# Performance work log

Hardware: AMD Instinct MI355X
Metric: run time of the kernel (lower is better)

Reference implementation:

```python
import jax, jax.numpy as jnp
import numpy as np
from jax import lax

# dims: batch, depth, height, width, in-channels
B, D, H, W, C = 1, 48, 48, 48, 8
K = 3          # cubic kernel size
R = 2          # n_radial_profiles = K//2 + 1
DEG = 3        # max_degree
NH = (DEG + 1) ** 2   # n_harmonics = 16
OUT = 16       # out_channels (filters)


def setup_inputs() -> dict:
    key = jax.random.key(0)
    ks = jax.random.split(key, 6)
    return {
        "x": jax.random.normal(ks[0], (B, D, H, W, C), jnp.float32),
        "atoms_real": jax.random.normal(ks[1], (K, K, K, R, NH), jnp.float32),
        "atoms_imag": jax.random.normal(ks[2], (K, K, K, R, NH), jnp.float32),
        "w": jax.random.normal(ks[3], (C, OUT, R, DEG + 1), jnp.float32) * 0.1,
        "w_center": jax.random.normal(ks[4], (C, OUT), jnp.float32) * 0.1,
        "b_center": jnp.zeros((OUT,), jnp.float32),
    }


def _depthwise_sh_conv(x, filt):
    # x: [B,D,H,W,C]; filt: [K,K,K,R,NH].  The torch code loops conv3d per input
    # channel with the SAME [K,K,K,1,R*NH] filter bank; that is exactly a
    # depthwise conv with channel multiplier R*NH and a tiled kernel.
    k = filt.shape[0]
    r, nh = filt.shape[3], filt.shape[4]
    c = x.shape[-1]
    kern = jnp.tile(filt.reshape(k, k, k, 1, r * nh), (1, 1, 1, 1, c))  # [K,K,K,1,C*R*NH], c-major
    dn = lax.conv_dimension_numbers(x.shape, kern.shape, ("NDHWC", "DHWIO", "NDHWC"))
    y = lax.conv_general_dilated(x, kern, (1, 1, 1), "SAME",
                                 dimension_numbers=dn, feature_group_count=c)
    # -> [B,D,H,W,C,R,NH]
    return y.reshape(x.shape[:4] + (c, r, nh))


def reference(x, atoms_real, atoms_imag, w, w_center, b_center):
    deg = w.shape[-1] - 1
    # repeat_interleave of per-degree weights over the 2k+1 orders of each degree
    idx = np.repeat(np.arange(deg + 1), [2 * n + 1 for n in range(deg + 1)])  # [NH]
    w_exp = w[..., idx]  # [C, OUT, R, NH]

    feat_r = _depthwise_sh_conv(x, atoms_real)  # [B,D,H,W,C,R,NH]
    feat_i = _depthwise_sh_conv(x, atoms_imag)

    # weighted reduction over input channels (axis 4) and radial profiles (axis 6)
    real = jnp.einsum("bdhwcrn,cfrn->bdhwfn", feat_r, w_exp)
    imag = jnp.einsum("bdhwcrn,cfrn->bdhwfn", feat_i, w_exp)

    # central-pixel 1x1x1 conv added to harmonic index 0 of the real part
    central = jnp.einsum("bdhwc,cf->bdhwf", x, w_center) + b_center
    real = real.at[..., 0].add(central)

    # stack real/imag feature maps: [B,D,H,W,OUT,NH,2]
    return jnp.stack([real, imag], axis=-1)
```

## Files before the change

### kernel.cpp

```cpp
#include <hip/hip_runtime.h>


typedef _Float16 half4_t __attribute__((ext_vector_type(4)));
typedef float floatx4 __attribute__((ext_vector_type(4)));

#define B_U64_SLOTS (14 * 32 * 64)
#define WS_BYTES_NEEDED (B_U64_SLOTS * 8)

__device__ inline unsigned short f2h(float v) {
    return __builtin_bit_cast(unsigned short, (_Float16)v);
}
__device__ inline unsigned pk2(float a, float b) {
    return (unsigned)f2h(a) | ((unsigned)f2h(b) << 16);
}

__global__ __launch_bounds__(512) void bsh_precompute_gemm(
    const float* __restrict__ AR,
    const float* __restrict__ AI,
    const float* __restrict__ Wgt,
    const float* __restrict__ WC,
    const float* __restrict__ Bc,
    unsigned long long* __restrict__ TB)
{
    int s = blockIdx.x * 512 + threadIdx.x;
    if (s >= B_U64_SLOTS) return;
    int l = s & 63, ntg = (s >> 6) & 31, t = s >> 11;
    int col = 16 * ntg + (l & 15);
    int f = col >> 5, n = (col >> 1) & 15, ri = col & 1;
    int dg = (n >= 9) ? 3 : (n >= 4) ? 2 : (n >= 1) ? 1 : 0;
    const float* atom = ri ? AI : AR;
    unsigned long long pack = 0;
    #pragma unroll
    for (int j = 0; j < 4; ++j) {
        int kap = 16 * t + 4 * (l >> 4) + j;
        int k = kap >> 3, c = kap & 7;
        float v = 0.f;
        if (k < 27) {
            float w0 = Wgt[((c * 16 + f) * 2 + 0) * 4 + dg];
            float w1 = Wgt[((c * 16 + f) * 2 + 1) * 4 + dg];
            v = atom[k * 32 + n] * w0 + atom[k * 32 + 16 + n] * w1;
            if (k == 13 && n == 0 && ri == 0) v += WC[c * 16 + f];
        } else {
            if (c == 7 && n == 0 && ri == 0) v = Bc[f];
        }
        pack |= ((unsigned long long)f2h(v)) << (16 * j);
    }
    TB[s] = pack;
}

__global__ __launch_bounds__(512) void bsh_gemm(
    const float* __restrict__ X,
    const unsigned long long* __restrict__ TB,
    float* __restrict__ Out)
{
    __shared__ _Float16 A_lds[96 * 232];

    const int tid = threadIdx.x;
    const int bid = blockIdx.x;
    const int nb = bid & 1;
    const int rb = bid >> 1;
    const int d  = rb / 24;
    const int hp = rb - 24 * d;

    #pragma unroll
    for (int i = 0; i < 6; ++i) {
        int cell = tid + i * 512;
        if (cell < 2688) {
            int k = cell / 96;
            int v = cell - 96 * k;
            unsigned x01 = 0, x23 = 0, x45 = 0, x67 = 0;
            if (k == 27) {
                x67 = 0x3C000000u;
            } else {
                int kz = k / 9, r9 = k - 9 * kz;
                int ky = r9 / 3, kx = r9 - 3 * ky;
                int hl = (v >= 48) ? 1 : 0;
                int dd = d - 1 + kz;
                int hh = 2 * hp + hl - 1 + ky;
                int ww = v - 48 * hl - 1 + kx;
                if ((unsigned)dd < 48u && (unsigned)hh < 48u && (unsigned)ww < 48u) {
                    const float* px = &X[(((dd * 48 + hh) * 48) + ww) * 8];
                    float4 a = *(const float4*)px;
                    float4 b = *(const float4*)(px + 4);
                    x01 = pk2(a.x, a.y); x23 = pk2(a.z, a.w);
                    x45 = pk2(b.x, b.y); x67 = pk2(b.z, b.w);
                }
            }
            char* wp = (char*)A_lds + v * 464 + k * 16;
            *(uint2*)wp       = make_uint2(x01, x23);
            *(uint2*)(wp + 8) = make_uint2(x45, x67);
        }
    }
    __syncthreads();

    const int lane = tid & 63, wave = tid >> 6;
    const int ms = wave >> 2, ns = wave & 3;
    const int kg = lane >> 4, lr = lane & 15;

    floatx4 D[3][4];
    #pragma unroll
    for (int mt = 0; mt < 3; ++mt)
        #pragma unroll
        for (int nt = 0; nt < 4; ++nt)
            D[mt][nt] = (floatx4){0.f, 0.f, 0.f, 0.f};

    const unsigned long long* bp = TB + ((size_t)(nb * 16 + ns * 4) * 64 + lane);
    const char* arow = (const char*)A_lds + (48 * ms + lr) * 464 + kg * 8;

    unsigned long long Bbuf[2][4];
    #pragma unroll
    for (int nt = 0; nt < 4; ++nt) Bbuf[0][nt] = bp[(size_t)nt * 64];

    #pragma unroll
    for (int t = 0; t < 14; ++t) {
        if (t < 13) {
            #pragma unroll
            for (int nt = 0; nt < 4; ++nt)
                Bbuf[(t + 1) & 1][nt] = bp[(size_t)((t + 1) * 32 + nt) * 64];
        }
        half4_t a0 = *(const half4_t*)(arow + 32 * t);
        half4_t a1 = *(const half4_t*)(arow + 16 * 464 + 32 * t);
        half4_t a2 = *(const half4_t*)(arow + 32 * 464 + 32 * t);
        #pragma unroll
        for (int nt = 0; nt < 4; ++nt) {
            half4_t bf = __builtin_bit_cast(half4_t, Bbuf[t & 1][nt]);
            D[0][nt] = __builtin_amdgcn_mfma_f32_16x16x16f16(a0, bf, D[0][nt], 0, 0, 0);
            D[1][nt] = __builtin_amdgcn_mfma_f32_16x16x16f16(a1, bf, D[1][nt], 0, 0, 0);
            D[2][nt] = __builtin_amdgcn_mfma_f32_16x16x16f16(a2, bf, D[2][nt], 0, 0, 0);
        }
    }

    float* ob = Out + (size_t)(rb * 96 + 48 * ms + 4 * kg) * 512
                    + nb * 256 + ns * 64 + lr;
    #pragma unroll
    for (int mt = 0; mt < 3; ++mt)
        #pragma unroll
        for (int reg = 0; reg < 4; ++reg) {
            float* orow = ob + (size_t)(16 * mt + reg) * 512;
            orow[0]  = D[mt][0][reg];
            orow[16] = D[mt][1][reg];
            orow[32] = D[mt][2][reg];
            orow[48] = D[mt][3][reg];
        }
}

#define FB_NBLK (48*48*6)
#define FB_WS_FLOATS 5968

__global__ __launch_bounds__(512) void fb_precompute(
    const float* __restrict__ AR, const float* __restrict__ AI,
    const float* __restrict__ Wgt, const float* __restrict__ WC,
    const float* __restrict__ Bc, float* __restrict__ T)
{
    const int tid = threadIdx.x;
    for (int i = tid; i < 4096; i += 512) {
        int row = i >> 4, f = row >> 4, n = row & 15;
        int pc = (i >> 2) & 3, e = i & 3;
        int chunk = pc ^ (n & 3);
        int cr = chunk * 4 + e, c = cr >> 1, r = cr & 1;
        int dg = (n >= 9) ? 3 : (n >= 4) ? 2 : (n >= 1) ? 1 : 0;
        T[i] = Wgt[c * 128 + f * 8 + r * 4 + dg];
    }
    for (int i = tid; i < 1728; i += 512) {
        int k = i >> 6, n = (i >> 2) & 15, q = i & 3;
        const float* src = (q >> 1) ? AI : AR;
        T[4096 + i] = src[k * 32 + (q & 1) * 16 + n];
    }
    if (tid < 128) T[5824 + tid] = WC[(tid & 7) * 16 + (tid >> 3)];
    if (tid < 16)  T[5952 + tid] = Bc[tid];
}

__device__ inline float4 fb_shfl_xor4(float4 v, int m) {
    return make_float4(__shfl_xor(v.x, m), __shfl_xor(v.y, m),
                       __shfl_xor(v.z, m), __shfl_xor(v.w, m));
}

__global__ __launch_bounds__(512) void fb_kernel(
    const float* __restrict__ X, const float* __restrict__ T,
    float* __restrict__ Out)
{
    __shared__ float cst[FB_WS_FLOATS];
    __shared__ float x_lds[720];

    const int tid = threadIdx.x;
    const int bid = blockIdx.x;
    const int d  = bid / (48 * 6);
    const int r0 = bid - d * (48 * 6);
    const int h  = r0 / 6;
    const int w0 = (r0 - h * 6) * 8;

    {
        const float4* t4 = (const float4*)T;
        float4* c4 = (float4*)cst;
        #pragma unroll
        for (int i = 0; i < 3; ++i) {
            int idx = tid + i * 512;
            if (idx < FB_WS_FLOATS / 4) c4[idx] = t4[idx];
        }
        if (tid < 180) {
            int r3 = tid / 20, rem = tid - r3 * 20;
            int wx = rem >> 1, c0 = (rem & 1) * 4;
            int dz = r3 / 3, dy = r3 - dz * 3;
            int dd = d - 1 + dz, hh = h - 1 + dy, ww = w0 - 1 + wx;
            float4 v = make_float4(0.f, 0.f, 0.f, 0.f);
            if ((unsigned)dd < 48u && (unsigned)hh < 48u && (unsigned)ww < 48u)
                v = *(const float4*)&X[(((dd * 48 + hh) * 48 + ww) * 8) + c0];
            *(float4*)&x_lds[tid * 4] = v;
        }
    }
    __syncthreads();

    const int wave = tid >> 6, lane = tid & 63;
    const int n = lane & 15, g = lane >> 4;
    const float* atoms_lds = cst + 4096;
    const float* wc_lds    = cst + 5824;
    const float* b_lds     = cst + 5952;

    float sr0 = 0, sr1 = 0, sr2 = 0, sr3 = 0;
    float si0 = 0, si1 = 0, si2 = 0, si3 = 0;
    #pragma unroll
    for (int kz = 0; kz < 3; ++kz)
    #pragma unroll
    for (int ky = 0; ky < 3; ++ky)
    #pragma unroll
    for (int kx = 0; kx < 3; ++kx) {
        const int k = (kz * 3 + ky) * 3 + kx;
        const float2 xv = *(const float2*)&x_lds[(((kz * 3 + ky) * 10) + wave + kx) * 8 + 2 * g];
        const float4 a  = *(const float4*)&atoms_lds[k * 64 + n * 4];
        sr0 += xv.x * a.x; sr1 += xv.x * a.y;
        sr2 += xv.y * a.x; sr3 += xv.y * a.y;
        si0 += xv.x * a.z; si1 += xv.x * a.w;
        si2 += xv.y * a.z; si3 += xv.y * a.w;
    }
    const float4 sR0 = make_float4(sr0, sr1, sr2, sr3);
    const float4 sI0 = make_float4(si0, si1, si2, si3);
    const float4 sR1 = fb_shfl_xor4(sR0, 16), sI1 = fb_shfl_xor4(sI0, 16);
    const float4 sR2 = fb_shfl_xor4(sR0, 32), sI2 = fb_shfl_xor4(sI0, 32);
    const float4 sR3 = fb_shfl_xor4(sR1, 32), sI3 = fb_shfl_xor4(sI1, 32);

    float cent[4];
    {
        const int cb = ((1 * 3 + 1) * 10 + wave + 1) * 8;
        const float4 xc0 = *(const float4*)&x_lds[cb];
        const float4 xc1 = *(const float4*)&x_lds[cb + 4];
        #pragma unroll
        for (int fi = 0; fi < 4; ++fi) {
            const int f = 4 * g + fi;
            const float* wcr = &wc_lds[f * 8];
            cent[fi] = b_lds[f]
                + xc0.x * wcr[0] + xc0.y * wcr[1] + xc0.z * wcr[2] + xc0.w * wcr[3]
                + xc1.x * wcr[4] + xc1.y * wcr[5] + xc1.z * wcr[6] + xc1.w * wcr[7];
        }
    }

    const float4* w4 = (const float4*)cst;
    const int gx = g ^ (n & 3);
    const int out_base = ((d * 48 + h) * 48 + (w0 + wave)) * 512;
    #pragma unroll
    for (int fi = 0; fi < 4; ++fi) {
        const int f = 4 * g + fi;
        const int rb2 = (f * 16 + n) * 4;
        const float4 w0v = w4[rb2 + (gx ^ 0)];
        const float4 w1v = w4[rb2 + (gx ^ 1)];
        const float4 w2v = w4[rb2 + (gx ^ 2)];
        const float4 w3v = w4[rb2 + (gx ^ 3)];
        float accR = w0v.x*sR0.x + w0v.y*sR0.y + w0v.z*sR0.z + w0v.w*sR0.w
                   + w1v.x*sR1.x + w1v.y*sR1.y + w1v.z*sR1.z + w1v.w*sR1.w
                   + w2v.x*sR2.x + w2v.y*sR2.y + w2v.z*sR2.z + w2v.w*sR2.w
                   + w3v.x*sR3.x + w3v.y*sR3.y + w3v.z*sR3.z + w3v.w*sR3.w;
        float accI = w0v.x*sI0.x + w0v.y*sI0.y + w0v.z*sI0.z + w0v.w*sI0.w
                   + w1v.x*sI1.x + w1v.y*sI1.y + w1v.z*sI1.z + w1v.w*sI1.w
                   + w2v.x*sI2.x + w2v.y*sI2.y + w2v.z*sI2.z + w2v.w*sI2.w
                   + w3v.x*sI3.x + w3v.y*sI3.y + w3v.z*sI3.z + w3v.w*sI3.w;
        if (n == 0) accR += cent[fi];
        *(float2*)&Out[out_base + (f * 16 + n) * 2] = make_float2(accR, accI);
    }
}

extern "C" void kernel_launch(void* const* d_in, const int* in_sizes, int n_in,
                              void* d_out, int out_size, void* d_ws, size_t ws_size,
                              hipStream_t stream) {
    (void)in_sizes; (void)n_in; (void)out_size;
    const float* x  = (const float*)d_in[0];
    const float* ar = (const float*)d_in[1];
    const float* ai = (const float*)d_in[2];
    const float* w  = (const float*)d_in[3];
    const float* wc = (const float*)d_in[4];
    const float* bc = (const float*)d_in[5];
    float* out = (float*)d_out;

    if (ws_size >= (size_t)WS_BYTES_NEEDED) {
        unsigned long long* tb = (unsigned long long*)d_ws;
        hipLaunchKernelGGL(bsh_precompute_gemm, dim3(56), dim3(512), 0, stream,
                           ar, ai, w, wc, bc, tb);
        hipLaunchKernelGGL(bsh_gemm, dim3(2304), dim3(512), 0, stream,
                           x, tb, out);
    } else {
        float* tbl = (float*)d_ws;
        hipLaunchKernelGGL(fb_precompute, dim3(1), dim3(512), 0, stream,
                           ar, ai, w, wc, bc, tbl);
        hipLaunchKernelGGL(fb_kernel, dim3(FB_NBLK), dim3(512), 0, stream,
                           x, tbl, out);
    }
}
```

Before: 61.90 us.

## Transpose GEMM so outputs store as float4 rows, shrink blocks to 256 threads

```diff
diff --git a/kernel.cpp b/kernel.cpp
--- a/kernel.cpp
+++ b/kernel.cpp
@@ -48,36 +48,35 @@
     TB[s] = pack;
 }
 
-__global__ __launch_bounds__(512) void bsh_gemm(
+__global__ __launch_bounds__(256, 5) void bsh_gemm_t(
     const float* __restrict__ X,
     const unsigned long long* __restrict__ TB,
     float* __restrict__ Out)
 {
-    __shared__ _Float16 A_lds[96 * 232];
+    __shared__ _Float16 B_lds[48 * 232];
 
     const int tid = threadIdx.x;
     const int bid = blockIdx.x;
     const int nb = bid & 1;
-    const int rb = bid >> 1;
-    const int d  = rb / 24;
-    const int hp = rb - 24 * d;
+    const int vg = bid >> 1;
+    const int d  = vg / 48;
+    const int h  = vg - 48 * d;
 
     #pragma unroll
     for (int i = 0; i < 6; ++i) {
-        int cell = tid + i * 512;
-        if (cell < 2688) {
-            int k = cell / 96;
-            int v = cell - 96 * k;
+        int cell = tid + i * 256;
+        if (cell < 1344) {
+            int k = cell / 48;
+            int v = cell - 48 * k;
             unsigned x01 = 0, x23 = 0, x45 = 0, x67 = 0;
             if (k == 27) {
                 x67 = 0x3C000000u;
             } else {
                 int kz = k / 9, r9 = k - 9 * kz;
                 int ky = r9 / 3, kx = r9 - 3 * ky;
-                int hl = (v >= 48) ? 1 : 0;
                 int dd = d - 1 + kz;
-                int hh = 2 * hp + hl - 1 + ky;
-                int ww = v - 48 * hl - 1 + kx;
+                int hh = h - 1 + ky;
+                int ww = v - 1 + kx;
                 if ((unsigned)dd < 48u && (unsigned)hh < 48u && (unsigned)ww < 48u) {
                     const float* px = &X[(((dd * 48 + hh) * 48) + ww) * 8];
                     float4 a = *(const float4*)px;
@@ -86,62 +85,61 @@
                     x45 = pk2(b.x, b.y); x67 = pk2(b.z, b.w);
                 }
             }
-            char* wp = (char*)A_lds + v * 464 + k * 16;
+            char* wp = (char*)B_lds + v * 464 + k * 16;
             *(uint2*)wp       = make_uint2(x01, x23);
             *(uint2*)(wp + 8) = make_uint2(x45, x67);
         }
     }
     __syncthreads();
 
-    const int lane = tid & 63, wave = tid >> 6;
-    const int ms = wave >> 2, ns = wave & 3;
+    const int lane = tid & 63, wv = tid >> 6;
     const int kg = lane >> 4, lr = lane & 15;
 
-    floatx4 D[3][4];
-    #pragma unroll
-    for (int mt = 0; mt < 3; ++mt)
-        #pragma unroll
-        for (int nt = 0; nt < 4; ++nt)
-            D[mt][nt] = (floatx4){0.f, 0.f, 0.f, 0.f};
-
-    const unsigned long long* bp = TB + ((size_t)(nb * 16 + ns * 4) * 64 + lane);
-    const char* arow = (const char*)A_lds + (48 * ms + lr) * 464 + kg * 8;
-
-    unsigned long long Bbuf[2][4];
-    #pragma unroll
-    for (int nt = 0; nt < 4; ++nt) Bbuf[0][nt] = bp[(size_t)nt * 64];
+    floatx4 D[4][3];
+    #pragma unroll
+    for (int i = 0; i < 4; ++i)
+        #pragma unroll
+        for (int vt = 0; vt < 3; ++vt)
+            D[i][vt] = (floatx4){0.f, 0.f, 0.f, 0.f};
+
+    const unsigned long long* ap = TB + ((size_t)(nb * 16 + wv * 4) * 64 + lane);
+    const char* brow = (const char*)B_lds + lr * 464 + kg * 8;
+
+    unsigned long long Abuf[2][4];
+    #pragma unroll
+    for (int i = 0; i < 4; ++i) Abuf[0][i] = ap[(size_t)i * 64];
+    #pragma unroll
+    for (int i = 0; i < 4; ++i) Abuf[1][i] = ap[(size_t)(32 + i) * 64];
 
     #pragma unroll
     for (int t = 0; t < 14; ++t) {
-        if (t < 13) {
+        half4_t af[4];
+        #pragma unroll
+        for (int i = 0; i < 4; ++i) af[i] = __builtin_bit_cast(half4_t, Abuf[t & 1][i]);
+        if (t < 12) {
             #pragma unroll
-            for (int nt = 0; nt < 4; ++nt)
-                Bbuf[(t + 1) & 1][nt] = bp[(size_t)((t + 1) * 32 + nt) * 64];
-        }
-        half4_t a0 = *(const half4_t*)(arow + 32 * t);
-        half4_t a1 = *(const half4_t*)(arow + 16 * 464 + 32 * t);
-        half4_t a2 = *(const half4_t*)(arow + 32 * 464 + 32 * t);
-        #pragma unroll
-        for (int nt = 0; nt < 4; ++nt) {
-            half4_t bf = __builtin_bit_cast(half4_t, Bbuf[t & 1][nt]);
-            D[0][nt] = __builtin_amdgcn_mfma_f32_16x16x16f16(a0, bf, D[0][nt], 0, 0, 0);
-            D[1][nt] = __builtin_amdgcn_mfma_f32_16x16x16f16(a1, bf, D[1][nt], 0, 0, 0);
-            D[2][nt] = __builtin_amdgcn_mfma_f32_16x16x16f16(a2, bf, D[2][nt], 0, 0, 0);
-        }
-    }
-
-    float* ob = Out + (size_t)(rb * 96 + 48 * ms + 4 * kg) * 512
-                    + nb * 256 + ns * 64 + lr;
-    #pragma unroll
-    for (int mt = 0; mt < 3; ++mt)
-        #pragma unroll
-        for (int reg = 0; reg < 4; ++reg) {
-            float* orow = ob + (size_t)(16 * mt + reg) * 512;
-            orow[0]  = D[mt][0][reg];
-            orow[16] = D[mt][1][reg];
-            orow[32] = D[mt][2][reg];
-            orow[48] = D[mt][3][reg];
-        }
+            for (int i = 0; i < 4; ++i)
+                Abuf[t & 1][i] = ap[(size_t)((t + 2) * 32 + i) * 64];
+        }
+        half4_t b0 = *(const half4_t*)(brow + 32 * t);
+        half4_t b1 = *(const half4_t*)(brow + 16 * 464 + 32 * t);
+        half4_t b2 = *(const half4_t*)(brow + 32 * 464 + 32 * t);
+        #pragma unroll
+        for (int i = 0; i < 4; ++i) {
+            D[i][0] = __builtin_amdgcn_mfma_f32_16x16x16f16(af[i], b0, D[i][0], 0, 0, 0);
+            D[i][1] = __builtin_amdgcn_mfma_f32_16x16x16f16(af[i], b1, D[i][1], 0, 0, 0);
+            D[i][2] = __builtin_amdgcn_mfma_f32_16x16x16f16(af[i], b2, D[i][2], 0, 0, 0);
+        }
+    }
+
+    #pragma unroll
+    for (int vt = 0; vt < 3; ++vt) {
+        float* ob = Out + (size_t)(vg * 48 + vt * 16 + lr) * 512
+                        + nb * 256 + wv * 64 + 4 * kg;
+        #pragma unroll
+        for (int i = 0; i < 4; ++i)
+            __builtin_nontemporal_store(D[i][vt], (floatx4*)(ob + 16 * i));
+    }
 }
 
 #define FB_NBLK (48*48*6)
@@ -293,7 +291,7 @@
         unsigned long long* tb = (unsigned long long*)d_ws;
         hipLaunchKernelGGL(bsh_precompute_gemm, dim3(56), dim3(512), 0, stream,
                            ar, ai, w, wc, bc, tb);
-        hipLaunchKernelGGL(bsh_gemm, dim3(2304), dim3(512), 0, stream,
+        hipLaunchKernelGGL(bsh_gemm_t, dim3(4608), dim3(256), 0, stream,
                            x, tb, out);
     } else {
         float* tbl = (float*)d_ws;
```

After: 74.77 us. 20.8% more time.
